# Performance work log

Hardware: AMD Instinct MI355X
Metric: run time of the kernel (lower is better)

Reference implementation:

```python
import jax, jax.numpy as jnp
import numpy as np

C = 512
NUM_HEADS = 8
HEAD_DIM = C // NUM_HEADS


def setup_inputs() -> dict:
    key = jax.random.key(0)
    ks = jax.random.split(key, 9)
    s = 1.0 / np.sqrt(C)
    x = jax.random.normal(ks[0], (8, C, 32, 32), dtype=jnp.float32)
    Wq = jax.random.uniform(ks[1], (C, C), jnp.float32, -s, s)
    bq = jax.random.uniform(ks[2], (C,), jnp.float32, -s, s)
    Wk = jax.random.uniform(ks[3], (C, C), jnp.float32, -s, s)
    bk = jax.random.uniform(ks[4], (C,), jnp.float32, -s, s)
    Wv = jax.random.uniform(ks[5], (C, C), jnp.float32, -s, s)
    bv = jax.random.uniform(ks[6], (C,), jnp.float32, -s, s)
    Wo = jax.random.uniform(ks[7], (C, C), jnp.float32, -s, s)
    bo = jax.random.uniform(ks[8], (C,), jnp.float32, -s, s)
    return {"x": x, "Wq": Wq, "bq": bq, "Wk": Wk, "bk": bk,
            "Wv": Wv, "bv": bv, "Wo": Wo, "bo": bo}


def reference(x, Wq, bq, Wk, bk, Wv, bv, Wo, bo):
    N, Cc, H, W = x.shape
    S = H * W
    # [N, S, C] token sequence
    xs = x.reshape(N, Cc, S).transpose(0, 2, 1)
    # torch Linear: y = x @ W^T + b
    q = xs @ Wq.T + bq
    k = xs @ Wk.T + bk
    v = xs @ Wv.T + bv
    # [N, h, S, d]
    q = q.reshape(N, S, NUM_HEADS, HEAD_DIM).transpose(0, 2, 1, 3)
    k = k.reshape(N, S, NUM_HEADS, HEAD_DIM).transpose(0, 2, 1, 3)
    v = v.reshape(N, S, NUM_HEADS, HEAD_DIM).transpose(0, 2, 1, 3)
    energy = jnp.einsum('nhqd,nhkd->nhqk', q, k)
    attn = jax.nn.softmax(energy / np.sqrt(HEAD_DIM), axis=3)
    out = jnp.einsum('nhql,nhld->nhqd', attn, v)
    # back to [N, S, C]; note torch reshape from (N,h,S,d) order
    out = out.reshape(N, Cc, S) if False else out.reshape(N, -1, Cc)
    out = out @ Wo.T + bo
    return out.reshape(N, Cc, H, W)


if __name__ == "__main__":
    o = reference(**setup_inputs())
    print(o.shape)
```

## Files before the change

kernel.cpp:

```cpp
#include <hip/hip_runtime.h>


typedef _Float16 f16x8 __attribute__((ext_vector_type(8)));
typedef _Float16 f16x4 __attribute__((ext_vector_type(4)));
typedef float f32x4 __attribute__((ext_vector_type(4)));

__device__ inline void gl_lds16(const void* g, void* l) {
  __builtin_amdgcn_global_load_lds((const __attribute__((address_space(1))) void*)g,
                                   (__attribute__((address_space(3))) void*)l, 16, 0, 0);
}

__device__ inline float fexp2(float x) {
#if __has_builtin(__builtin_amdgcn_exp2f)
  return __builtin_amdgcn_exp2f(x);
#else
  return exp2f(x);
#endif
}

__global__ void prep(const float* __restrict__ x,
                     const float* __restrict__ Wq, const float* __restrict__ bq,
                     const float* __restrict__ Wk, const float* __restrict__ bk,
                     const float* __restrict__ Wv, const float* __restrict__ bv,
                     const float* __restrict__ Wo,
                     _Float16* __restrict__ xs16, _Float16* __restrict__ Wqkv16,
                     float* __restrict__ bqkv, _Float16* __restrict__ Wo16) {
  __shared__ float t[32][33];
  const int tid = threadIdx.x;
  if (blockIdx.x < 1024) {
    const float g = 0.18033688011112042f;
    int i = blockIdx.x * 256 + tid;
    Wqkv16[i]          = (_Float16)(Wq[i] * g);
    Wqkv16[262144 + i] = (_Float16)Wk[i];
    Wqkv16[524288 + i] = (_Float16)Wv[i];
    Wo16[i]            = (_Float16)Wo[i];
    if (i < 512) {
      bqkv[i]        = bq[i] * g;
      bqkv[512 + i]  = bk[i];
      bqkv[1024 + i] = bv[i];
    }
    return;
  }
  const int bid2 = blockIdx.x - 1024;
  const int n = bid2 & 7;
  const int r = bid2 >> 3;
  const int c0 = ((r >> 5) & 15) * 32, s0 = (r & 31) * 32;
  const int tx = tid & 31, ty = tid >> 5;
#pragma unroll
  for (int i = 0; i < 4; ++i) {
    int cc = ty + i * 8;
    t[cc][tx] = x[((size_t)n * 512 + c0 + cc) * 1024 + s0 + tx];
  }
  __syncthreads();
#pragma unroll
  for (int i = 0; i < 4; ++i) {
    int ss = ty + i * 8;
    xs16[((size_t)n * 1024 + s0 + ss) * 512 + c0 + tx] = (_Float16)t[tx][ss];
  }
}

__global__ __launch_bounds__(256, 2) void qkv_gemm(
    const _Float16* __restrict__ A, const _Float16* __restrict__ Bw,
    const float* __restrict__ bias, _Float16* __restrict__ QK,
    _Float16* __restrict__ Vt) {
  __shared__ _Float16 smem[16896];
  _Float16* As = smem;
  _Float16* Bs = smem + 8192;
  const int tid = threadIdx.x;
  const int lane = tid & 63, w = tid >> 6;
  const int quad = lane >> 4, l15 = lane & 15;
  const int id = blockIdx.x;
  const int xcd = id & 7, k = id >> 3;
  const int bm = (xcd * 8 + (k & 7)) * 128;
  const int bnt = k >> 3;
  const int bn = bnt * 128;
  const int wr = (w >> 1) * 64, wc = (w & 1) * 64;
  f32x4 acc[4][4] = {};
  for (int k0 = 0; k0 < 512; k0 += 64) {
    __syncthreads();
#pragma unroll
    for (int c = 0; c < 4; ++c) {
      int idx = c * 256 + tid;
      int row = idx >> 3, sc = idx & 7;
      int kg = sc ^ (row & 7);
      gl_lds16(A + (size_t)(bm + row) * 512 + k0 + kg * 8, As + idx * 8);
      gl_lds16(Bw + (size_t)(bn + row) * 512 + k0 + kg * 8, Bs + idx * 8);
    }
    __syncthreads();
#pragma unroll
    for (int kh = 0; kh < 2; ++kh) {
      f16x8 af[4], bf[4];
#pragma unroll
      for (int i = 0; i < 4; ++i) {
        int ra = wr + i * 16 + l15;
        af[i] = *(const f16x8*)(As + ra * 64 + ((kh * 4 + quad) ^ (ra & 7)) * 8);
        int rb = wc + i * 16 + l15;
        bf[i] = *(const f16x8*)(Bs + rb * 64 + ((kh * 4 + quad) ^ (rb & 7)) * 8);
      }
#pragma unroll
      for (int i = 0; i < 4; ++i)
#pragma unroll
        for (int j = 0; j < 4; ++j)
          acc[i][j] = __builtin_amdgcn_mfma_f32_16x16x32_f16(af[i], bf[j], acc[i][j], 0, 0, 0);
    }
  }
  if (bnt < 8) {
#pragma unroll
    for (int j = 0; j < 4; ++j) {
      int col = bn + wc + j * 16 + l15;
      float bb = bias[col];
#pragma unroll
      for (int i = 0; i < 4; ++i) {
        int rowb = bm + wr + i * 16 + quad * 4;
#pragma unroll
        for (int r = 0; r < 4; ++r)
          QK[(size_t)(rowb + r) * 1024 + col] = (_Float16)(acc[i][j][r] + bb);
      }
    }
  } else {
    __syncthreads();
#pragma unroll
    for (int j = 0; j < 4; ++j) {
      int cl = wc + j * 16 + l15;
      float bb = bias[bn + cl];
#pragma unroll
      for (int i = 0; i < 4; ++i) {
        int row = wr + i * 16 + quad * 4;
        f16x4 pk;
#pragma unroll
        for (int r = 0; r < 4; ++r) pk[r] = (_Float16)(acc[i][j][r] + bb);
        *(f16x4*)(smem + cl * 132 + row) = pk;
      }
    }
    __syncthreads();
    const int n = bm >> 10, s0g = bm & 1023;
    const int vh = (bn - 1024) >> 6;
    const int cl = tid >> 1, par = tid & 1;
    const int hh = vh + (cl >> 6), d = cl & 63;
    const size_t vrow = (((size_t)((n * 8 + hh) * 64 + d)) << 10) + s0g;
#pragma unroll
    for (int g = 0; g < 8; ++g) {
      int pb = g * 16 + par * 8;
      int a32 = pb & ~31, q = (pb >> 3) & 3;
      f16x4 lo = *(const f16x4*)(smem + cl * 132 + a32 + 4 * q);
      f16x4 hi = *(const f16x4*)(smem + cl * 132 + a32 + 16 + 4 * q);
      f16x8 o = {lo[0], lo[1], lo[2], lo[3], hi[0], hi[1], hi[2], hi[3]};
      *(f16x8*)(Vt + vrow + pb) = o;
    }
  }
}

__global__ __launch_bounds__(256, 2) void attn(
    const _Float16* __restrict__ QK, const _Float16* __restrict__ Vt,
    _Float16* __restrict__ O16) {
  __shared__ _Float16 Qs[128 * 64];
  __shared__ _Float16 Ks[128 * 64];
  __shared__ _Float16 Vs[64 * 128];
  const int tid = threadIdx.x, lane = tid & 63, w = tid >> 6;
  const int quad = lane >> 4, l15 = lane & 15;
  const int id = blockIdx.x;
  const int n = id & 7, h = (id >> 3) & 7;
  const int q0 = (id >> 6) * 128;
#pragma unroll
  for (int c = 0; c < 4; ++c) {
    int idx = c * 256 + tid;
    int row = idx >> 3, sc = idx & 7;
    int dg = sc ^ (row & 7);
    gl_lds16(QK + (size_t)(n * 1024 + q0 + row) * 1024 + h * 64 + dg * 8, Qs + idx * 8);
  }
  __syncthreads();
  f16x8 qf[2][2];
#pragma unroll
  for (int mt = 0; mt < 2; ++mt)
#pragma unroll
    for (int dc = 0; dc < 2; ++dc) {
      int row = w * 32 + mt * 16 + l15;
      qf[mt][dc] = *(const f16x8*)(Qs + row * 64 + ((dc * 4 + quad) ^ (row & 7)) * 8);
    }
  f32x4 oaccT[4][2] = {};
  f32x4 lsum[2] = {};
  const f16x8 ones = {(_Float16)1, (_Float16)1, (_Float16)1, (_Float16)1,
                      (_Float16)1, (_Float16)1, (_Float16)1, (_Float16)1};

  for (int kt = 0; kt < 8; ++kt) {
    __syncthreads();
#pragma unroll
    for (int c = 0; c < 4; ++c) {
      int idx = c * 256 + tid;
      int row = idx >> 3, sck = idx & 7;
      int dg = sck ^ (row & 7);
      gl_lds16(QK + (size_t)(n * 1024 + kt * 128 + row) * 1024 + 512 + h * 64 + dg * 8,
               Ks + idx * 8);
      int d = idx >> 4, scv = idx & 15;
      int vg = scv ^ (d & 7);
      gl_lds16(Vt + (size_t)((n * 8 + h) * 64 + d) * 1024 + kt * 128 + vg * 8,
               Vs + idx * 8);
    }
    __syncthreads();
#pragma unroll
    for (int sc = 0; sc < 4; ++sc) {
      f32x4 sacc[2][2] = {};
#pragma unroll
      for (int t = 0; t < 2; ++t) {
        int rk = (sc * 2 + t) * 16 + l15;
        f16x8 kf0 = *(const f16x8*)(Ks + rk * 64 + ((quad) ^ (rk & 7)) * 8);
        f16x8 kf1 = *(const f16x8*)(Ks + rk * 64 + ((4 + quad) ^ (rk & 7)) * 8);
#pragma unroll
        for (int mt = 0; mt < 2; ++mt) {
          sacc[mt][t] = __builtin_amdgcn_mfma_f32_16x16x32_f16(kf0, qf[mt][0], sacc[mt][t], 0, 0, 0);
          sacc[mt][t] = __builtin_amdgcn_mfma_f32_16x16x32_f16(kf1, qf[mt][1], sacc[mt][t], 0, 0, 0);
        }
      }
      f16x8 pf[2];
#pragma unroll
      for (int mt = 0; mt < 2; ++mt) {
#pragma unroll
        for (int t = 0; t < 2; ++t)
#pragma unroll
          for (int r = 0; r < 4; ++r)
            pf[mt][t * 4 + r] = (_Float16)fexp2(sacc[mt][t][r]);
        lsum[mt] = __builtin_amdgcn_mfma_f32_16x16x32_f16(pf[mt], ones, lsum[mt], 0, 0, 0);
      }
#pragma unroll
      for (int nt = 0; nt < 4; ++nt) {
        int rd = nt * 16 + l15;
        f16x8 vf = *(const f16x8*)(Vs + rd * 128 + ((sc * 4 + quad) ^ (rd & 7)) * 8);
#pragma unroll
        for (int mt = 0; mt < 2; ++mt)
          oaccT[nt][mt] = __builtin_amdgcn_mfma_f32_16x16x32_f16(vf, pf[mt], oaccT[nt][mt], 0, 0, 0);
      }
    }
  }
#pragma unroll
  for (int mt = 0; mt < 2; ++mt) {
    int r3 = l15 & 3;
    float lv = lsum[mt][0];
    lv = (r3 == 1) ? lsum[mt][1] : lv;
    lv = (r3 == 2) ? lsum[mt][2] : lv;
    lv = (r3 == 3) ? lsum[mt][3] : lv;
    float lq = __shfl(lv, (l15 >> 2) * 16 + (l15 & 3), 64);
    float rinv = 1.0f / lq;
    int q = q0 + w * 32 + mt * 16 + l15;
    int i = h * 128 + (q >> 3);
    size_t base = (size_t)(n * 1024 + i) * 512 + (q & 7) * 64 + quad * 4;
#pragma unroll
    for (int nt = 0; nt < 4; ++nt) {
      f16x4 pk;
#pragma unroll
      for (int r = 0; r < 4; ++r) pk[r] = (_Float16)(oaccT[nt][mt][r] * rinv);
      *(f16x4*)(O16 + base + nt * 16) = pk;
    }
  }
}

__global__ __launch_bounds__(256, 2) void out_gemm(
    const _Float16* __restrict__ A, const _Float16* __restrict__ Bw,
    const float* __restrict__ bias, float* __restrict__ out) {
  __shared__ _Float16 As[128 * 32];
  __shared__ _Float16 Bs[128 * 32];
  const int tid = threadIdx.x;
  const int lane = tid & 63, w = tid >> 6;
  const int quad = lane >> 4, l15 = lane & 15;
  const int id = blockIdx.x;
  const int xcd = id & 7, k = id >> 3;
  const int bm = (xcd * 8 + (k & 7)) * 128;
  const int bn = (k >> 3) * 128;
  const int wr = (w >> 1) * 64, wc = (w & 1) * 64;
  f32x4 acc[4][4] = {};
  for (int k0 = 0; k0 < 512; k0 += 32) {
    __syncthreads();
#pragma unroll
    for (int c = 0; c < 2; ++c) {
      int idx = c * 256 + tid;
      int row = idx >> 2, sc = idx & 3;
      int kg = sc ^ ((row >> 1) & 3);
      gl_lds16(A + (size_t)(bm + row) * 512 + k0 + kg * 8, As + idx * 8);
      gl_lds16(Bw + (size_t)(bn + row) * 512 + k0 + kg * 8, Bs + idx * 8);
    }
    __syncthreads();
    f16x8 af[4], bf[4];
#pragma unroll
    for (int i = 0; i < 4; ++i) {
      int ra = wr + i * 16 + l15;
      af[i] = *(const f16x8*)(As + ra * 32 + (quad ^ ((ra >> 1) & 3)) * 8);
      int rb = wc + i * 16 + l15;
      bf[i] = *(const f16x8*)(Bs + rb * 32 + (quad ^ ((rb >> 1) & 3)) * 8);
    }
#pragma unroll
    for (int i = 0; i < 4; ++i)
#pragma unroll
      for (int j = 0; j < 4; ++j)
        acc[i][j] = __builtin_amdgcn_mfma_f32_16x16x32_f16(af[i], bf[j], acc[i][j], 0, 0, 0);
  }
#pragma unroll
  for (int j = 0; j < 4; ++j) {
    int col = bn + wc + j * 16 + l15;
    float bb = bias[col];
#pragma unroll
    for (int i = 0; i < 4; ++i) {
      int rowb = bm + wr + i * 16 + quad * 4;
#pragma unroll
      for (int r = 0; r < 4; ++r)
        out[(size_t)(rowb + r) * 512 + col] = acc[i][j][r] + bb;
    }
  }
}

extern "C" void kernel_launch(void* const* d_in, const int* in_sizes, int n_in,
                              void* d_out, int out_size, void* d_ws, size_t ws_size,
                              hipStream_t stream) {
  const float* x  = (const float*)d_in[0];
  const float* Wq = (const float*)d_in[1];
  const float* bq = (const float*)d_in[2];
  const float* Wk = (const float*)d_in[3];
  const float* bk = (const float*)d_in[4];
  const float* Wv = (const float*)d_in[5];
  const float* bv = (const float*)d_in[6];
  const float* Wo = (const float*)d_in[7];
  const float* bo = (const float*)d_in[8];
  float* out = (float*)d_out;
  char* ws = (char*)d_ws;

  _Float16* xs16   = (_Float16*)(ws);
  _Float16* QK     = (_Float16*)(ws + (8u << 20));
  _Float16* Vt     = (_Float16*)(ws + (24u << 20));
  _Float16* Wqkv16 = (_Float16*)(ws + (32u << 20));
  _Float16* Wo16   = (_Float16*)(ws + (32u << 20) + 1572864);
  float*    bqkv   = (float*)   (ws + (32u << 20) + 2097152);

  hipLaunchKernelGGL(prep, dim3(5120), dim3(256), 0, stream,
                     x, Wq, bq, Wk, bk, Wv, bv, Wo, xs16, Wqkv16, bqkv, Wo16);
  hipLaunchKernelGGL(qkv_gemm, dim3(768), dim3(256), 0, stream,
                     xs16, Wqkv16, bqkv, QK, Vt);
  hipLaunchKernelGGL(attn, dim3(512), dim3(256), 0, stream, QK, Vt, xs16);
  hipLaunchKernelGGL(out_gemm, dim3(256), dim3(256), 0, stream,
                     xs16, Wo16, bo, out);
}
```

Measured before the change: 134.6 us.

## Double-buffer LDS tiles in QKV, attention and output GEMM kernels

Converts the QKV GEMM, attention and output GEMM kernels to double-buffered LDS. Each iteration issues the global-to-LDS loads for the next tile before computing on the current one, with a single barrier per iteration. The QKV GEMM also drops from 64-wide to 32-wide K tiles. The attention kernel now loads Q fragments directly from global memory instead of staging them through LDS. The aim is to hide global load latency behind MFMA work. The cost is more LDS per block, which may reduce occupancy, and possibly uncoalesced direct Q loads.

```diff
diff --git a/kernel.cpp b/kernel.cpp
--- a/kernel.cpp
+++ b/kernel.cpp
@@ -64,8 +64,6 @@
     const float* __restrict__ bias, _Float16* __restrict__ QK,
     _Float16* __restrict__ Vt) {
   __shared__ _Float16 smem[16896];
-  _Float16* As = smem;
-  _Float16* Bs = smem + 8192;
   const int tid = threadIdx.x;
   const int lane = tid & 63, w = tid >> 6;
   const int quad = lane >> 4, l15 = lane & 15;
@@ -75,34 +73,46 @@
   const int bnt = k >> 3;
   const int bn = bnt * 128;
   const int wr = (w >> 1) * 64, wc = (w & 1) * 64;
+  const int srow = (tid * 2) >> 2, ssc0 = (tid * 2) & 3;
   f32x4 acc[4][4] = {};
-  for (int k0 = 0; k0 < 512; k0 += 64) {
+#pragma unroll
+  for (int c = 0; c < 2; ++c) {
+    int idx = c * 256 + tid;
+    int row = idx >> 2, sc = idx & 3;
+    int kg = sc ^ ((row >> 1) & 3);
+    gl_lds16(A + (size_t)(bm + row) * 512 + kg * 8, smem + idx * 8);
+    gl_lds16(Bw + (size_t)(bn + row) * 512 + kg * 8, smem + 4096 + idx * 8);
+  }
+  __syncthreads();
+  for (int ki = 0; ki < 16; ++ki) {
+    _Float16* As = smem + (ki & 1) * 8192;
+    _Float16* Bs = As + 4096;
+    if (ki < 15) {
+      _Float16* Asn = smem + ((ki + 1) & 1) * 8192;
+      int k0 = (ki + 1) * 32;
+#pragma unroll
+      for (int c = 0; c < 2; ++c) {
+        int idx = c * 256 + tid;
+        int row = idx >> 2, sc = idx & 3;
+        int kg = sc ^ ((row >> 1) & 3);
+        gl_lds16(A + (size_t)(bm + row) * 512 + k0 + kg * 8, Asn + idx * 8);
+        gl_lds16(Bw + (size_t)(bn + row) * 512 + k0 + kg * 8, Asn + 4096 + idx * 8);
+      }
+    }
+    f16x8 af[4], bf[4];
+#pragma unroll
+    for (int i = 0; i < 4; ++i) {
+      int ra = wr + i * 16 + l15;
+      af[i] = *(const f16x8*)(As + ra * 32 + (quad ^ ((ra >> 1) & 3)) * 8);
+      int rb = wc + i * 16 + l15;
+      bf[i] = *(const f16x8*)(Bs + rb * 32 + (quad ^ ((rb >> 1) & 3)) * 8);
+    }
+#pragma unroll
+    for (int i = 0; i < 4; ++i)
+#pragma unroll
+      for (int j = 0; j < 4; ++j)
+        acc[i][j] = __builtin_amdgcn_mfma_f32_16x16x32_f16(af[i], bf[j], acc[i][j], 0, 0, 0);
     __syncthreads();
-#pragma unroll
-    for (int c = 0; c < 4; ++c) {
-      int idx = c * 256 + tid;
-      int row = idx >> 3, sc = idx & 7;
-      int kg = sc ^ (row & 7);
-      gl_lds16(A + (size_t)(bm + row) * 512 + k0 + kg * 8, As + idx * 8);
-      gl_lds16(Bw + (size_t)(bn + row) * 512 + k0 + kg * 8, Bs + idx * 8);
-    }
-    __syncthreads();
-#pragma unroll
-    for (int kh = 0; kh < 2; ++kh) {
-      f16x8 af[4], bf[4];
-#pragma unroll
-      for (int i = 0; i < 4; ++i) {
-        int ra = wr + i * 16 + l15;
-        af[i] = *(const f16x8*)(As + ra * 64 + ((kh * 4 + quad) ^ (ra & 7)) * 8);
-        int rb = wc + i * 16 + l15;
-        bf[i] = *(const f16x8*)(Bs + rb * 64 + ((kh * 4 + quad) ^ (rb & 7)) * 8);
-      }
-#pragma unroll
-      for (int i = 0; i < 4; ++i)
-#pragma unroll
-        for (int j = 0; j < 4; ++j)
-          acc[i][j] = __builtin_amdgcn_mfma_f32_16x16x32_f16(af[i], bf[j], acc[i][j], 0, 0, 0);
-    }
   }
   if (bnt < 8) {
 #pragma unroll
@@ -118,7 +128,6 @@
       }
     }
   } else {
-    __syncthreads();
 #pragma unroll
     for (int j = 0; j < 4; ++j) {
       int cl = wc + j * 16 + l15;
@@ -153,9 +162,7 @@
 __global__ __launch_bounds__(256, 2) void attn(
     const _Float16* __restrict__ QK, const _Float16* __restrict__ Vt,
     _Float16* __restrict__ O16) {
-  __shared__ _Float16 Qs[128 * 64];
-  __shared__ _Float16 Ks[128 * 64];
-  __shared__ _Float16 Vs[64 * 128];
+  __shared__ _Float16 KV[2][16384];
   const int tid = threadIdx.x, lane = tid & 63, w = tid >> 6;
   const int quad = lane >> 4, l15 = lane & 15;
   const int id = blockIdx.x;
@@ -164,39 +171,48 @@
 #pragma unroll
   for (int c = 0; c < 4; ++c) {
     int idx = c * 256 + tid;
-    int row = idx >> 3, sc = idx & 7;
-    int dg = sc ^ (row & 7);
-    gl_lds16(QK + (size_t)(n * 1024 + q0 + row) * 1024 + h * 64 + dg * 8, Qs + idx * 8);
-  }
-  __syncthreads();
+    int row = idx >> 3, sck = idx & 7;
+    int dg = sck ^ (row & 7);
+    gl_lds16(QK + (size_t)(n * 1024 + row) * 1024 + 512 + h * 64 + dg * 8,
+             &KV[0][idx * 8]);
+    int d = idx >> 4, scv = idx & 15;
+    int vg = scv ^ (d & 7);
+    gl_lds16(Vt + (size_t)((n * 8 + h) * 64 + d) * 1024 + vg * 8,
+             &KV[0][8192 + idx * 8]);
+  }
   f16x8 qf[2][2];
 #pragma unroll
   for (int mt = 0; mt < 2; ++mt)
 #pragma unroll
     for (int dc = 0; dc < 2; ++dc) {
       int row = w * 32 + mt * 16 + l15;
-      qf[mt][dc] = *(const f16x8*)(Qs + row * 64 + ((dc * 4 + quad) ^ (row & 7)) * 8);
-    }
+      qf[mt][dc] = *(const f16x8*)(QK + (size_t)(n * 1024 + q0 + row) * 1024 +
+                                   h * 64 + (dc * 4 + quad) * 8);
+    }
+  __syncthreads();
   f32x4 oaccT[4][2] = {};
   f32x4 lsum[2] = {};
   const f16x8 ones = {(_Float16)1, (_Float16)1, (_Float16)1, (_Float16)1,
                       (_Float16)1, (_Float16)1, (_Float16)1, (_Float16)1};
 
   for (int kt = 0; kt < 8; ++kt) {
-    __syncthreads();
-#pragma unroll
-    for (int c = 0; c < 4; ++c) {
-      int idx = c * 256 + tid;
-      int row = idx >> 3, sck = idx & 7;
-      int dg = sck ^ (row & 7);
-      gl_lds16(QK + (size_t)(n * 1024 + kt * 128 + row) * 1024 + 512 + h * 64 + dg * 8,
-               Ks + idx * 8);
-      int d = idx >> 4, scv = idx & 15;
-      int vg = scv ^ (d & 7);
-      gl_lds16(Vt + (size_t)((n * 8 + h) * 64 + d) * 1024 + kt * 128 + vg * 8,
-               Vs + idx * 8);
-    }
-    __syncthreads();
+    const _Float16* Ks = &KV[kt & 1][0];
+    const _Float16* Vs = &KV[kt & 1][8192];
+    if (kt < 7) {
+      _Float16* nb = &KV[(kt + 1) & 1][0];
+#pragma unroll
+      for (int c = 0; c < 4; ++c) {
+        int idx = c * 256 + tid;
+        int row = idx >> 3, sck = idx & 7;
+        int dg = sck ^ (row & 7);
+        gl_lds16(QK + (size_t)(n * 1024 + (kt + 1) * 128 + row) * 1024 + 512 + h * 64 + dg * 8,
+                 nb + idx * 8);
+        int d = idx >> 4, scv = idx & 15;
+        int vg = scv ^ (d & 7);
+        gl_lds16(Vt + (size_t)((n * 8 + h) * 64 + d) * 1024 + (kt + 1) * 128 + vg * 8,
+                 nb + 8192 + idx * 8);
+      }
+    }
 #pragma unroll
     for (int sc = 0; sc < 4; ++sc) {
       f32x4 sacc[2][2] = {};
@@ -230,6 +246,7 @@
           oaccT[nt][mt] = __builtin_amdgcn_mfma_f32_16x16x32_f16(vf, pf[mt], oaccT[nt][mt], 0, 0, 0);
       }
     }
+    __syncthreads();
   }
 #pragma unroll
   for (int mt = 0; mt < 2; ++mt) {
@@ -256,8 +273,7 @@
 __global__ __launch_bounds__(256, 2) void out_gemm(
     const _Float16* __restrict__ A, const _Float16* __restrict__ Bw,
     const float* __restrict__ bias, float* __restrict__ out) {
-  __shared__ _Float16 As[128 * 32];
-  __shared__ _Float16 Bs[128 * 32];
+  __shared__ _Float16 smem[16384];
   const int tid = threadIdx.x;
   const int lane = tid & 63, w = tid >> 6;
   const int quad = lane >> 4, l15 = lane & 15;
@@ -267,17 +283,30 @@
   const int bn = (k >> 3) * 128;
   const int wr = (w >> 1) * 64, wc = (w & 1) * 64;
   f32x4 acc[4][4] = {};
-  for (int k0 = 0; k0 < 512; k0 += 32) {
-    __syncthreads();
-#pragma unroll
-    for (int c = 0; c < 2; ++c) {
-      int idx = c * 256 + tid;
-      int row = idx >> 2, sc = idx & 3;
-      int kg = sc ^ ((row >> 1) & 3);
-      gl_lds16(A + (size_t)(bm + row) * 512 + k0 + kg * 8, As + idx * 8);
-      gl_lds16(Bw + (size_t)(bn + row) * 512 + k0 + kg * 8, Bs + idx * 8);
-    }
-    __syncthreads();
+#pragma unroll
+  for (int c = 0; c < 2; ++c) {
+    int idx = c * 256 + tid;
+    int row = idx >> 2, sc = idx & 3;
+    int kg = sc ^ ((row >> 1) & 3);
+    gl_lds16(A + (size_t)(bm + row) * 512 + kg * 8, smem + idx * 8);
+    gl_lds16(Bw + (size_t)(bn + row) * 512 + kg * 8, smem + 4096 + idx * 8);
+  }
+  __syncthreads();
+  for (int ki = 0; ki < 16; ++ki) {
+    _Float16* As = smem + (ki & 1) * 8192;
+    _Float16* Bs = As + 4096;
+    if (ki < 15) {
+      _Float16* Asn = smem + ((ki + 1) & 1) * 8192;
+      int k0 = (ki + 1) * 32;
+#pragma unroll
+      for (int c = 0; c < 2; ++c) {
+        int idx = c * 256 + tid;
+        int row = idx >> 2, sc = idx & 3;
+        int kg = sc ^ ((row >> 1) & 3);
+        gl_lds16(A + (size_t)(bm + row) * 512 + k0 + kg * 8, Asn + idx * 8);
+        gl_lds16(Bw + (size_t)(bn + row) * 512 + k0 + kg * 8, Asn + 4096 + idx * 8);
+      }
+    }
     f16x8 af[4], bf[4];
 #pragma unroll
     for (int i = 0; i < 4; ++i) {
@@ -291,6 +320,7 @@
 #pragma unroll
       for (int j = 0; j < 4; ++j)
         acc[i][j] = __builtin_amdgcn_mfma_f32_16x16x32_f16(af[i], bf[j], acc[i][j], 0, 0, 0);
+    __syncthreads();
   }
 #pragma unroll
   for (int j = 0; j < 4; ++j) {
```

Measured after the change: 135.9 us. No clear change (+1.0%).
